# Kernel optimization log

Measured on AMD Instinct MI355X. Metric: run time of the kernel, lower is better.

Reference implementation:

```python
import jax, jax.numpy as jnp
import numpy as np

EMB_DIM = 1024
NUM_HEADS = 16
DEPTH = EMB_DIM // NUM_HEADS
B, LQ, LKV = 2, 1024, 2048


def setup_inputs() -> dict:
    key = jax.random.key(0)
    ks = jax.random.split(key, 8)
    s = 1.0 / np.sqrt(EMB_DIM)
    return {
        "x": jax.random.normal(ks[0], (B, LQ, EMB_DIM), jnp.float32),
        "context": jax.random.normal(ks[1], (B, LKV, EMB_DIM), jnp.float32),
        "pad_mask": jax.random.bernoulli(ks[2], 0.1, (B, LQ, LKV)),
        "Wq": jax.random.normal(ks[3], (EMB_DIM, EMB_DIM), jnp.float32) * s,
        "Wk": jax.random.normal(ks[4], (EMB_DIM, EMB_DIM), jnp.float32) * s,
        "Wv": jax.random.normal(ks[5], (EMB_DIM, EMB_DIM), jnp.float32) * s,
        "fc_w": jax.random.normal(ks[6], (EMB_DIM, EMB_DIM), jnp.float32) * s,
        "fc_b": jax.random.normal(ks[7], (EMB_DIM,), jnp.float32) * s,
    }


def reference(x, context, pad_mask, Wq, Wk, Wv, fc_w, fc_b):
    # Projections (torch Linear: y = x @ W.T)
    Q = jnp.einsum("bqe,fe->bqf", x, Wq)
    K = jnp.einsum("bke,fe->bkf", context, Wk)
    V = jnp.einsum("bke,fe->bkf", context, Wv)
    # Split heads: [B, H, L, D]
    Q = Q.reshape(B, LQ, NUM_HEADS, DEPTH).transpose(0, 2, 1, 3)
    K = K.reshape(B, LKV, NUM_HEADS, DEPTH).transpose(0, 2, 1, 3)
    V = V.reshape(B, LKV, NUM_HEADS, DEPTH).transpose(0, 2, 1, 3)
    # Scaled dot-product attention scores [B, H, LQ, LKV]
    scores = jnp.einsum("bhqd,bhkd->bhqk", Q, K) / np.sqrt(DEPTH).astype(np.float32)
    scores = jnp.where(pad_mask[:, None, :, :], jnp.float32(-1e9), scores)
    att = jax.nn.softmax(scores, axis=-1)
    out = jnp.einsum("bhqk,bhkd->bhqd", att, V)
    out = out.transpose(0, 2, 1, 3).reshape(B, LQ, EMB_DIM)
    return jnp.einsum("bqe,fe->bqf", out, fc_w) + fc_b
```

## Files before the change

kernel.cpp:

```cpp
#include <hip/hip_runtime.h>
#include <hip/hip_bf16.h>

#define B_   2
#define H_   16
#define LQ_  1024
#define LKV_ 2048
#define D_   64
#define E_   1024

typedef __attribute__((ext_vector_type(8))) _Float16 f16x8;
typedef __attribute__((ext_vector_type(4))) float   f32x4;

__device__ __forceinline__ void gload16_lds(const void* g, void* l) {
    __builtin_amdgcn_global_load_lds(
        (const __attribute__((address_space(1))) unsigned int*)g,
        (__attribute__((address_space(3))) unsigned int*)l, 16, 0, 0);
}

__global__ void probe16(const void* __restrict__ msk, int* __restrict__ modep) {
    int lane = threadIdx.x;
    int notInt = 0, notF32 = 0, notBF = 0;
    for (int i = lane; i < 256; i += 64) {
        unsigned v = ((const unsigned*)msk)[i * 997];
        if (v > 1u) notInt = 1;
        if (v != 0u && v != 0x3F800000u) notF32 = 1;
        if (v != 0u && v != 0x3F80u && v != 0x3F800000u && v != 0x3F803F80u) notBF = 1;
    }
    notInt = __any(notInt); notF32 = __any(notF32); notBF = __any(notBF);
    if (lane == 0) *modep = !notInt ? 0 : (!notF32 ? 1 : (!notBF ? 2 : 3));
}

__global__ void canon16_all(
    const float* __restrict__ x,  const float* __restrict__ ctx,
    const float* __restrict__ wq, const float* __restrict__ wk,
    const float* __restrict__ wv, const float* __restrict__ fw,
    const float* __restrict__ fb, const void* __restrict__ msk,
    _Float16* __restrict__ xh,  _Float16* __restrict__ ch,
    _Float16* __restrict__ wqh, _Float16* __restrict__ wkvh,
    _Float16* __restrict__ fwh, float* __restrict__ fbf,
    unsigned long long* __restrict__ Mbt, const int* __restrict__ modep)
{
    const int mmode = *modep;
    const int total = 1376384;
    const int stride = gridDim.x * blockDim.x;
    for (int idx = blockIdx.x * blockDim.x + threadIdx.x; idx < total; idx += stride) {
        if (idx < 1310720) {
            const float* src; _Float16* dst; int rel;
            if (idx < 262144)       { src = x;   dst = xh;   rel = idx; }
            else if (idx < 786432)  { src = ctx; dst = ch;   rel = idx - 262144; }
            else if (idx < 917504)  { src = wq;  dst = wqh;  rel = idx - 786432; }
            else if (idx < 1048576) { src = wk;  dst = wkvh; rel = idx - 917504; }
            else if (idx < 1179648) { src = wv;  dst = wkvh + (size_t)E_ * E_; rel = idx - 1048576; }
            else                    { src = fw;  dst = fwh;  rel = idx - 1179648; }
            f32x4 a = ((const f32x4*)src)[2 * rel], b = ((const f32x4*)src)[2 * rel + 1];
            f16x8 o;
            o[0] = (_Float16)a.x; o[1] = (_Float16)a.y; o[2] = (_Float16)a.z; o[3] = (_Float16)a.w;
            o[4] = (_Float16)b.x; o[5] = (_Float16)b.y; o[6] = (_Float16)b.z; o[7] = (_Float16)b.w;
            ((f16x8*)dst)[rel] = o;
        } else if (idx < 1310848) {
            int rel = idx - 1310720;
#pragma unroll
            for (int j = 0; j < 8; ++j) fbf[rel * 8 + j] = fb[rel * 8 + j];
        } else {
            int rel = idx - 1310848;
            const size_t base = (size_t)rel * 64;
            unsigned long long v = 0;
            if (mmode == 0) {
                const int* p = (const int*)msk + base;
#pragma unroll
                for (int j = 0; j < 64; ++j) if (p[j] != 0) v |= 1ull << j;
            } else if (mmode == 1) {
                const float* p = (const float*)msk + base;
#pragma unroll
                for (int j = 0; j < 64; ++j) if (p[j] != 0.0f) v |= 1ull << j;
            } else if (mmode == 2) {
                const unsigned short* p = (const unsigned short*)msk + base;
#pragma unroll
                for (int j = 0; j < 64; ++j) if (p[j] != 0) v |= 1ull << j;
            } else {
                const unsigned char* p = (const unsigned char*)msk + base;
#pragma unroll
                for (int j = 0; j < 64; ++j) if (p[j] != 0) v |= 1ull << j;
            }
            Mbt[(rel & 31) * 2048 + (rel >> 5)] = v;
        }
    }
}

__global__ __launch_bounds__(256) void gemm16_qkv(
    const _Float16* __restrict__ xh, const _Float16* __restrict__ ch,
    const _Float16* __restrict__ wqh, const _Float16* __restrict__ wkvh,
    _Float16* __restrict__ Qh, _Float16* __restrict__ Kh, _Float16* __restrict__ Vt)
{
    __shared__ __align__(16) _Float16 As[2][128 * 64];
    __shared__ __align__(16) _Float16 Bs[2][128 * 64];

    const int bid = blockIdx.x;
    const bool isQ = bid < 128;
    const _Float16* A; const _Float16* W; int tm, tn;
    if (isQ) { A = xh; W = wqh; tm = bid >> 3; tn = bid & 7; }
    else     { int b2 = bid - 128; A = ch; W = wkvh; tm = b2 >> 4; tn = b2 & 15; }

    const int tid = threadIdx.x;
    const int w = tid >> 6, lane = tid & 63;
    const int g = lane >> 4, c = lane & 15;
    const int wr = w >> 1, wc = w & 1;
    const int rowS = lane >> 3, slot = lane & 7;
    const int stSwz = ((slot ^ (rowS & 7)) << 4);
    const int swz0 = ((g ^ (c & 7)) << 4);
    const int swz1 = (((4 + g) ^ (c & 7)) << 4);

    f32x4 acc[4][4];
#pragma unroll
    for (int i = 0; i < 4; i++)
#pragma unroll
        for (int j = 0; j < 4; j++) acc[i][j] = f32x4{0.f, 0.f, 0.f, 0.f};

    const size_t rowB = (size_t)E_ * 2;
    const char* gAbase = (const char*)A + (size_t)(tm * 128) * rowB;
    const char* gBbase = (const char*)W + (size_t)(tn * 128) * rowB;

#pragma unroll
    for (int j = 0; j < 4; ++j) {
        int rloc = w * 32 + j * 8 + rowS;
        gload16_lds(gAbase + (size_t)rloc * rowB + stSwz,
                    (char*)As[0] + (w * 32 + j * 8) * 128 + lane * 16);
        gload16_lds(gBbase + (size_t)rloc * rowB + stSwz,
                    (char*)Bs[0] + (w * 32 + j * 8) * 128 + lane * 16);
    }
    __syncthreads();

    for (int kt = 0; kt < 16; ++kt) {
        if (kt < 15) {
            const int nb = (kt + 1) & 1;
#pragma unroll
            for (int j = 0; j < 4; ++j) {
                int rloc = w * 32 + j * 8 + rowS;
                gload16_lds(gAbase + (size_t)rloc * rowB + (kt + 1) * 128 + stSwz,
                            (char*)As[nb] + (w * 32 + j * 8) * 128 + lane * 16);
                gload16_lds(gBbase + (size_t)rloc * rowB + (kt + 1) * 128 + stSwz,
                            (char*)Bs[nb] + (w * 32 + j * 8) * 128 + lane * 16);
            }
        }
        const int cb = kt & 1;

        f16x8 bF[4][2];
#pragma unroll
        for (int ni = 0; ni < 4; ni++) {
            const char* bp = (const char*)Bs[cb] + (wc * 64 + ni * 16 + c) * 128;
            bF[ni][0] = *(const f16x8*)(bp + swz0);
            bF[ni][1] = *(const f16x8*)(bp + swz1);
        }
#pragma unroll
        for (int mi = 0; mi < 4; mi++) {
            const char* ap = (const char*)As[cb] + (wr * 64 + mi * 16 + c) * 128;
            f16x8 a0 = *(const f16x8*)(ap + swz0);
            f16x8 a1 = *(const f16x8*)(ap + swz1);
#pragma unroll
            for (int ni = 0; ni < 4; ni++) {
                acc[mi][ni] = __builtin_amdgcn_mfma_f32_16x16x32_f16(a0, bF[ni][0], acc[mi][ni], 0, 0, 0);
                acc[mi][ni] = __builtin_amdgcn_mfma_f32_16x16x32_f16(a1, bF[ni][1], acc[mi][ni], 0, 0, 0);
            }
        }
        __syncthreads();
    }

#pragma unroll
    for (int mi = 0; mi < 4; mi++) {
#pragma unroll
        for (int ni = 0; ni < 4; ni++) {
#pragma unroll
            for (int r = 0; r < 4; r++) {
                int R  = tm * 128 + wr * 64 + mi * 16 + g * 4 + r;
                int Cc = tn * 128 + wc * 64 + ni * 16 + c;
                float v = acc[mi][ni][r];
                if (isQ) {
                    int b = R >> 10, q = R & 1023;
                    int h = Cc >> 6, d = Cc & 63;
                    Qh[((size_t)(b * H_ + h) * LQ_ + q) * D_ + d] = (_Float16)(v * 0.18033688011112042f);
                } else {
                    int b = R >> 11, k = R & 2047;
                    int isV = Cc >> 10, cc2 = Cc & 1023;
                    int h = cc2 >> 6, d = cc2 & 63;
                    if (!isV)
                        Kh[((size_t)(b * H_ + h) * LKV_ + k) * D_ + d] = (_Float16)v;
                    else {
                        size_t bh = (size_t)(b * H_ + h);
                        Vt[((bh * (LKV_ / 64) + (k >> 6)) * D_ + d) * 64 + (k & 63)] = (_Float16)v;
                    }
                }
            }
        }
    }
}

__global__ __launch_bounds__(256) void gemm16_fc(
    const _Float16* __restrict__ A, const _Float16* __restrict__ W,
    const float* __restrict__ bias, float* __restrict__ Cout)
{
    __shared__ __align__(16) _Float16 As[2][128 * 64];
    __shared__ __align__(16) _Float16 Bs[2][128 * 64];

    const int tm = blockIdx.x >> 3, tn = blockIdx.x & 7;
    const int tid = threadIdx.x;
    const int w = tid >> 6, lane = tid & 63;
    const int g = lane >> 4, c = lane & 15;
    const int wr = w >> 1, wc = w & 1;
    const int rowS = lane >> 3, slot = lane & 7;
    const int stSwz = ((slot ^ (rowS & 7)) << 4);
    const int swz0 = ((g ^ (c & 7)) << 4);
    const int swz1 = (((4 + g) ^ (c & 7)) << 4);

    f32x4 acc[4][4];
#pragma unroll
    for (int i = 0; i < 4; i++)
#pragma unroll
        for (int j = 0; j < 4; j++) acc[i][j] = f32x4{0.f, 0.f, 0.f, 0.f};

    const size_t rowB = (size_t)E_ * 2;
    const char* gAbase = (const char*)A + (size_t)(tm * 128) * rowB;
    const char* gBbase = (const char*)W + (size_t)(tn * 128) * rowB;

#pragma unroll
    for (int j = 0; j < 4; ++j) {
        int rloc = w * 32 + j * 8 + rowS;
        gload16_lds(gAbase + (size_t)rloc * rowB + stSwz,
                    (char*)As[0] + (w * 32 + j * 8) * 128 + lane * 16);
        gload16_lds(gBbase + (size_t)rloc * rowB + stSwz,
                    (char*)Bs[0] + (w * 32 + j * 8) * 128 + lane * 16);
    }
    __syncthreads();

    for (int kt = 0; kt < 16; ++kt) {
        if (kt < 15) {
            const int nb = (kt + 1) & 1;
#pragma unroll
            for (int j = 0; j < 4; ++j) {
                int rloc = w * 32 + j * 8 + rowS;
                gload16_lds(gAbase + (size_t)rloc * rowB + (kt + 1) * 128 + stSwz,
                            (char*)As[nb] + (w * 32 + j * 8) * 128 + lane * 16);
                gload16_lds(gBbase + (size_t)rloc * rowB + (kt + 1) * 128 + stSwz,
                            (char*)Bs[nb] + (w * 32 + j * 8) * 128 + lane * 16);
            }
        }
        const int cb = kt & 1;

        f16x8 bF[4][2];
#pragma unroll
        for (int ni = 0; ni < 4; ni++) {
            const char* bp = (const char*)Bs[cb] + (wc * 64 + ni * 16 + c) * 128;
            bF[ni][0] = *(const f16x8*)(bp + swz0);
            bF[ni][1] = *(const f16x8*)(bp + swz1);
        }
#pragma unroll
        for (int mi = 0; mi < 4; mi++) {
            const char* ap = (const char*)As[cb] + (wr * 64 + mi * 16 + c) * 128;
            f16x8 a0 = *(const f16x8*)(ap + swz0);
            f16x8 a1 = *(const f16x8*)(ap + swz1);
#pragma unroll
            for (int ni = 0; ni < 4; ni++) {
                acc[mi][ni] = __builtin_amdgcn_mfma_f32_16x16x32_f16(a0, bF[ni][0], acc[mi][ni], 0, 0, 0);
                acc[mi][ni] = __builtin_amdgcn_mfma_f32_16x16x32_f16(a1, bF[ni][1], acc[mi][ni], 0, 0, 0);
            }
        }
        __syncthreads();
    }

#pragma unroll
    for (int mi = 0; mi < 4; mi++)
#pragma unroll
        for (int ni = 0; ni < 4; ni++)
#pragma unroll
            for (int r = 0; r < 4; r++) {
                int R  = tm * 128 + wr * 64 + mi * 16 + g * 4 + r;
                int Cc = tn * 128 + wc * 64 + ni * 16 + c;
                Cout[(size_t)R * E_ + Cc] = acc[mi][ni][r] + bias[Cc];
            }
}

__global__ __launch_bounds__(512) void attn16_kernel(
    const _Float16* __restrict__ Qh,
    const _Float16* __restrict__ Kh,
    const _Float16* __restrict__ Vt,
    const unsigned long long* __restrict__ Mbt,
    _Float16* __restrict__ O)
{
    __shared__ __align__(16) char ldsraw[65536];

    const int bid0 = blockIdx.x;
    const int xcd = bid0 & 7, jj = bid0 >> 3;
    const int bh = xcd * 4 + (jj >> 4);
    const int qt = jj & 15;
    const int b = bh >> 4, h = bh & 15;
    const int tid = threadIdx.x;
    const int w = tid >> 6, lane = tid & 63;
    const int g = lane >> 4, c = lane & 15;
    const int ws = w >> 2, wq = w & 3;
    const int q0 = qt * 64 + wq * 16;

    char* half = ldsraw + ws * 32768;

    f16x8 qf[2];
#pragma unroll
    for (int ks = 0; ks < 2; ++ks)
        qf[ks] = *(const f16x8*)&Qh[((size_t)bh * LQ_ + q0 + c) * D_ + ks * 32 + g * 8];

    f32x4 o[4];
#pragma unroll
    for (int dt = 0; dt < 4; dt++) o[dt] = f32x4{0.f, 0.f, 0.f, 0.f};
    float m = -1e30f, lsum = 0.f;

    const int rowS = (lane >> 3);
    const int stOffBase = (rowS * 128) + (((lane & 7) ^ (rowS & 7)) * 16);
    const char* kTileB = (const char*)Kh + (size_t)bh * (LKV_ * D_ * 2) + (size_t)ws * 16 * 8192;
    const char* vTileB = (const char*)Vt + (size_t)bh * (LKV_ * D_ * 2) + (size_t)ws * 16 * 8192;

    int rdOff[2];
#pragma unroll
    for (int ks = 0; ks < 2; ++ks)
        rdOff[ks] = c * 128 + (((ks * 4 + g) ^ (c & 7)) * 16);

    const int srcLo = (((g & 1) << 1) * 16 + c) << 2;
    const int srcHi = ((((g & 1) << 1) + 1) * 16 + c) << 2;
    const bool hiSel = (g >= 2);

    const int mRowIdx = b * LQ_ + q0 + c;
    const size_t mTile0 = (size_t)(ws * 16) * 2048 + mRowIdx;

    {
#pragma unroll
        for (int j = 0; j < 2; ++j) {
            gload16_lds(kTileB + (wq * 2048 + j * 1024) + stOffBase, half + (wq * 2048 + j * 1024));
            gload16_lds(vTileB + (wq * 2048 + j * 1024) + stOffBase, half + 8192 + (wq * 2048 + j * 1024));
        }
    }
    __syncthreads();

    for (int t = 0; t < 16; ++t) {
        if (t < 15) {
            const char* kt = kTileB + (size_t)(t + 1) * 8192;
            const char* vt = vTileB + (size_t)(t + 1) * 8192;
            char* dst = half + ((t + 1) & 1) * 16384;
#pragma unroll
            for (int j = 0; j < 2; ++j) {
                gload16_lds(kt + (wq * 2048 + j * 1024) + stOffBase, dst + (wq * 2048 + j * 1024));
                gload16_lds(vt + (wq * 2048 + j * 1024) + stOffBase, dst + 8192 + (wq * 2048 + j * 1024));
            }
        }

        const char* bufp = half + (t & 1) * 16384;

        f32x4 s[4];
#pragma unroll
        for (int nt = 0; nt < 4; ++nt) {
            f32x4 accS = f32x4{0.f, 0.f, 0.f, 0.f};
#pragma unroll
            for (int ks = 0; ks < 2; ++ks) {
                f16x8 kf = *(const f16x8*)(bufp + nt * 2048 + rdOff[ks]);
                accS = __builtin_amdgcn_mfma_f32_16x16x32_f16(kf, qf[ks], accS, 0, 0, 0);
            }
            s[nt] = accS;
        }
        unsigned long long mks = Mbt[mTile0 + (size_t)t * 2048] >> (g * 4);
#pragma unroll
        for (int nt = 0; nt < 4; ++nt) {
            unsigned nib = (unsigned)(mks >> (nt * 16)) & 0xFu;
            if (nib & 1u) s[nt][0] = -1e9f;
            if (nib & 2u) s[nt][1] = -1e9f;
            if (nib & 4u) s[nt][2] = -1e9f;
            if (nib & 8u) s[nt][3] = -1e9f;
        }
        float t0 = fmaxf(fmaxf(s[0][0], s[0][1]), fmaxf(s[0][2], s[0][3]));
        float t1 = fmaxf(fmaxf(s[1][0], s[1][1]), fmaxf(s[1][2], s[1][3]));
        float t2 = fmaxf(fmaxf(s[2][0], s[2][1]), fmaxf(s[2][2], s[2][3]));
        float t3 = fmaxf(fmaxf(s[3][0], s[3][1]), fmaxf(s[3][2], s[3][3]));
        float tmax = fmaxf(fmaxf(t0, t1), fmaxf(t2, t3));
        tmax = fmaxf(tmax, __shfl_xor(tmax, 16, 64));
        tmax = fmaxf(tmax, __shfl_xor(tmax, 32, 64));
        if (!__all(tmax - m <= 8.0f)) {
            float mn = fmaxf(m, tmax);
            float scl = exp2f(m - mn);
            m = mn;
            lsum *= scl;
#pragma unroll
            for (int dt = 0; dt < 4; dt++)
#pragma unroll
                for (int r = 0; r < 4; r++) o[dt][r] *= scl;
        }
        float ts = 0.f;
#pragma unroll
        for (int nt = 0; nt < 4; ++nt) {
            float p0 = exp2f(s[nt][0] - m);
            float p1 = exp2f(s[nt][1] - m);
            float p2 = exp2f(s[nt][2] - m);
            float p3 = exp2f(s[nt][3] - m);
            s[nt][0] = p0; s[nt][1] = p1; s[nt][2] = p2; s[nt][3] = p3;
            ts += (p0 + p1) + (p2 + p3);
        }
        ts += __shfl_xor(ts, 16, 64);
        ts += __shfl_xor(ts, 32, 64);
        lsum += ts;
        int pk[4][2];
#pragma unroll
        for (int nt = 0; nt < 4; ++nt) {
            pk[nt][0] = __builtin_bit_cast(int, __builtin_amdgcn_cvt_pkrtz(s[nt][0], s[nt][1]));
            pk[nt][1] = __builtin_bit_cast(int, __builtin_amdgcn_cvt_pkrtz(s[nt][2], s[nt][3]));
        }
#pragma unroll
        for (int ks = 0; ks < 2; ++ks) {
            const int ntL = 2 * ks, ntH = 2 * ks + 1;
            int aL0 = __builtin_amdgcn_ds_bpermute(srcLo, pk[ntL][0]);
            int aL1 = __builtin_amdgcn_ds_bpermute(srcLo, pk[ntL][1]);
            int aH0 = __builtin_amdgcn_ds_bpermute(srcHi, pk[ntL][0]);
            int aH1 = __builtin_amdgcn_ds_bpermute(srcHi, pk[ntL][1]);
            int bL0 = __builtin_amdgcn_ds_bpermute(srcLo, pk[ntH][0]);
            int bL1 = __builtin_amdgcn_ds_bpermute(srcLo, pk[ntH][1]);
            int bH0 = __builtin_amdgcn_ds_bpermute(srcHi, pk[ntH][0]);
            int bH1 = __builtin_amdgcn_ds_bpermute(srcHi, pk[ntH][1]);
            int u[4];
            u[0] = hiSel ? bL0 : aL0;
            u[1] = hiSel ? bL1 : aL1;
            u[2] = hiSel ? bH0 : aH0;
            u[3] = hiSel ? bH1 : aH1;
            f16x8 pf;
            {
                union { int i[4]; f16x8 v; } cvt;
                cvt.i[0] = u[0]; cvt.i[1] = u[1]; cvt.i[2] = u[2]; cvt.i[3] = u[3];
                pf = cvt.v;
            }
#pragma unroll
            for (int dt = 0; dt < 4; ++dt) {
                f16x8 vf = *(const f16x8*)(bufp + 8192 + dt * 2048 + rdOff[ks]);
                o[dt] = __builtin_amdgcn_mfma_f32_16x16x32_f16(vf, pf, o[dt], 0, 0, 0);
            }
        }
        __syncthreads();
    }

    float* OfP = (float*)ldsraw;
    float* Ml  = (float*)(ldsraw + 34816);
#pragma unroll
    for (int dt = 0; dt < 4; ++dt)
#pragma unroll
        for (int r = 0; r < 4; r++)
            OfP[(w * 16 + c) * 68 + dt * 16 + 4 * g + r] = o[dt][r];
    if (lane < 16) {
        Ml[(w * 16 + lane) * 2 + 0] = m;
        Ml[(w * 16 + lane) * 2 + 1] = lsum;
    }
    __syncthreads();

    const int d = tid & 63;
    const int qlBase = tid >> 6;
#pragma unroll
    for (int pass = 0; pass < 8; ++pass) {
        int ql = pass * 8 + qlBase;
        float m0 = Ml[ql * 2], l0 = Ml[ql * 2 + 1];
        float m1 = Ml[(64 + ql) * 2], l1 = Ml[(64 + ql) * 2 + 1];
        float M  = fmaxf(m0, m1);
        float e0 = exp2f(m0 - M), e1 = exp2f(m1 - M);
        float L  = l0 * e0 + l1 * e1;
        float acc = OfP[ql * 68 + d] * e0 + OfP[(64 + ql) * 68 + d] * e1;
        O[((size_t)b * LQ_ + qt * 64 + ql) * E_ + h * 64 + d] = (_Float16)(acc / L);
    }
}

extern "C" void kernel_launch(void* const* d_in, const int* in_sizes, int n_in,
                              void* d_out, int out_size, void* d_ws, size_t ws_size,
                              hipStream_t stream)
{
    const float* x   = (const float*)d_in[0];
    const float* ctx = (const float*)d_in[1];
    const void*  msk = d_in[2];
    const float* Wq  = (const float*)d_in[3];
    const float* Wk  = (const float*)d_in[4];
    const float* Wv  = (const float*)d_in[5];
    const float* fcw = (const float*)d_in[6];
    const float* fcb = (const float*)d_in[7];
    float* out = (float*)d_out;

    char* ws = (char*)d_ws;
    size_t off = 0;
    auto alloc = [&](size_t bytes) { char* p = ws + off; off += (bytes + 255) & ~255ull; return p; };

    int* modep = (int*)alloc(256);
    unsigned long long* Mbt = (unsigned long long*)alloc((size_t)B_ * LQ_ * (LKV_ / 64) * 8);
    _Float16* xh   = (_Float16*)alloc((size_t)B_ * LQ_ * E_ * 2);
    _Float16* ch   = (_Float16*)alloc((size_t)B_ * LKV_ * E_ * 2);
    _Float16* wqh  = (_Float16*)alloc((size_t)E_ * E_ * 2);
    _Float16* wkvh = (_Float16*)alloc((size_t)2 * E_ * E_ * 2);
    _Float16* fwh  = (_Float16*)alloc((size_t)E_ * E_ * 2);
    float*    fbf  = (float*)alloc((size_t)E_ * 4);
    _Float16* Qh   = (_Float16*)alloc((size_t)B_ * H_ * LQ_ * D_ * 2);
    _Float16* Kh   = (_Float16*)alloc((size_t)B_ * H_ * LKV_ * D_ * 2);
    _Float16* Vt   = (_Float16*)alloc((size_t)B_ * H_ * LKV_ * D_ * 2);
    _Float16* Ob   = xh;
    (void)ws_size; (void)in_sizes; (void)n_in; (void)out_size;

    probe16<<<1, 64, 0, stream>>>(msk, modep);

    canon16_all<<<2048, 256, 0, stream>>>(x, ctx, Wq, Wk, Wv, fcw, fcb, msk,
                                          xh, ch, wqh, wkvh, fwh, fbf, Mbt, modep);

    gemm16_qkv<<<640, 256, 0, stream>>>(xh, ch, wqh, wkvh, Qh, Kh, Vt);

    attn16_kernel<<<512, 512, 0, stream>>>(Qh, Kh, Vt, Mbt, Ob);

    gemm16_fc<<<128, 256, 0, stream>>>(Ob, fwh, fbf, out);
}
```

Measured before the change: 143.1 us.

## Split attention KV range across separate blocks with global combine kernel

```diff
diff --git a/kernel.cpp b/kernel.cpp
--- a/kernel.cpp
+++ b/kernel.cpp
@@ -9,15 +9,25 @@
 #define E_   1024
 
 typedef __attribute__((ext_vector_type(8))) _Float16 f16x8;
+typedef __attribute__((ext_vector_type(4))) _Float16 f16x4;
 typedef __attribute__((ext_vector_type(4))) float   f32x4;
+typedef __attribute__((ext_vector_type(4))) unsigned short u16x4;
 
 __device__ __forceinline__ void gload16_lds(const void* g, void* l) {
     __builtin_amdgcn_global_load_lds(
         (const __attribute__((address_space(1))) unsigned int*)g,
         (__attribute__((address_space(3))) unsigned int*)l, 16, 0, 0);
 }
-
-__global__ void probe16(const void* __restrict__ msk, int* __restrict__ modep) {
+__device__ __forceinline__ unsigned short f2bf(float f) {
+    union { float f; unsigned u; } v; v.f = f;
+    unsigned r = v.u + 0x7FFFu + ((v.u >> 16) & 1u);
+    return (unsigned short)(r >> 16);
+}
+__device__ __forceinline__ float bf2f(unsigned short u) {
+    union { unsigned u; float f; } v; v.u = ((unsigned)u) << 16; return v.f;
+}
+
+__global__ void probe17(const void* __restrict__ msk, int* __restrict__ modep) {
     int lane = threadIdx.x;
     int notInt = 0, notF32 = 0, notBF = 0;
     for (int i = lane; i < 256; i += 64) {
@@ -30,7 +40,7 @@
     if (lane == 0) *modep = !notInt ? 0 : (!notF32 ? 1 : (!notBF ? 2 : 3));
 }
 
-__global__ void canon16_all(
+__global__ void canon17_all(
     const float* __restrict__ x,  const float* __restrict__ ctx,
     const float* __restrict__ wq, const float* __restrict__ wk,
     const float* __restrict__ wv, const float* __restrict__ fw,
@@ -87,7 +97,7 @@
     }
 }
 
-__global__ __launch_bounds__(256) void gemm16_qkv(
+__global__ __launch_bounds__(256) void gemm17_qkv(
     const _Float16* __restrict__ xh, const _Float16* __restrict__ ch,
     const _Float16* __restrict__ wqh, const _Float16* __restrict__ wkvh,
     _Float16* __restrict__ Qh, _Float16* __restrict__ Kh, _Float16* __restrict__ Vt)
@@ -194,7 +204,7 @@
     }
 }
 
-__global__ __launch_bounds__(256) void gemm16_fc(
+__global__ __launch_bounds__(256) void gemm17_fc(
     const _Float16* __restrict__ A, const _Float16* __restrict__ W,
     const float* __restrict__ bias, float* __restrict__ Cout)
 {
@@ -278,27 +288,26 @@
             }
 }
 
-__global__ __launch_bounds__(512) void attn16_kernel(
+__global__ __launch_bounds__(256) void attn17_kernel(
     const _Float16* __restrict__ Qh,
     const _Float16* __restrict__ Kh,
     const _Float16* __restrict__ Vt,
     const unsigned long long* __restrict__ Mbt,
-    _Float16* __restrict__ O)
+    unsigned short* __restrict__ Opart,
+    float* __restrict__ Ml2)
 {
-    __shared__ __align__(16) char ldsraw[65536];
+    __shared__ __align__(16) char ldsraw[32768];
 
     const int bid0 = blockIdx.x;
     const int xcd = bid0 & 7, jj = bid0 >> 3;
-    const int bh = xcd * 4 + (jj >> 4);
-    const int qt = jj & 15;
-    const int b = bh >> 4, h = bh & 15;
+    const int bh = xcd * 4 + (jj >> 5);
+    const int rem = jj & 31;
+    const int qt = rem >> 1, ksHalf = rem & 1;
+    const int b = bh >> 4, h = bh & 15; (void)h; (void)b;
     const int tid = threadIdx.x;
     const int w = tid >> 6, lane = tid & 63;
     const int g = lane >> 4, c = lane & 15;
-    const int ws = w >> 2, wq = w & 3;
-    const int q0 = qt * 64 + wq * 16;
-
-    char* half = ldsraw + ws * 32768;
+    const int q0 = qt * 64 + w * 16;
 
     f16x8 qf[2];
 #pragma unroll
@@ -312,8 +321,8 @@
 
     const int rowS = (lane >> 3);
     const int stOffBase = (rowS * 128) + (((lane & 7) ^ (rowS & 7)) * 16);
-    const char* kTileB = (const char*)Kh + (size_t)bh * (LKV_ * D_ * 2) + (size_t)ws * 16 * 8192;
-    const char* vTileB = (const char*)Vt + (size_t)bh * (LKV_ * D_ * 2) + (size_t)ws * 16 * 8192;
+    const char* kTileB = (const char*)Kh + (size_t)bh * (LKV_ * D_ * 2) + (size_t)ksHalf * 16 * 8192;
+    const char* vTileB = (const char*)Vt + (size_t)bh * (LKV_ * D_ * 2) + (size_t)ksHalf * 16 * 8192;
 
     int rdOff[2];
 #pragma unroll
@@ -324,14 +333,14 @@
     const int srcHi = ((((g & 1) << 1) + 1) * 16 + c) << 2;
     const bool hiSel = (g >= 2);
 
-    const int mRowIdx = b * LQ_ + q0 + c;
-    const size_t mTile0 = (size_t)(ws * 16) * 2048 + mRowIdx;
+    const int mRowIdx = (bh >> 4) * LQ_ + q0 + c;
+    const size_t mTile0 = (size_t)(ksHalf * 16) * 2048 + mRowIdx;
 
     {
 #pragma unroll
         for (int j = 0; j < 2; ++j) {
-            gload16_lds(kTileB + (wq * 2048 + j * 1024) + stOffBase, half + (wq * 2048 + j * 1024));
-            gload16_lds(vTileB + (wq * 2048 + j * 1024) + stOffBase, half + 8192 + (wq * 2048 + j * 1024));
+            gload16_lds(kTileB + (w * 2048 + j * 1024) + stOffBase, ldsraw + (w * 2048 + j * 1024));
+            gload16_lds(vTileB + (w * 2048 + j * 1024) + stOffBase, ldsraw + 8192 + (w * 2048 + j * 1024));
         }
     }
     __syncthreads();
@@ -340,15 +349,15 @@
         if (t < 15) {
             const char* kt = kTileB + (size_t)(t + 1) * 8192;
             const char* vt = vTileB + (size_t)(t + 1) * 8192;
-            char* dst = half + ((t + 1) & 1) * 16384;
+            char* dst = ldsraw + ((t + 1) & 1) * 16384;
 #pragma unroll
             for (int j = 0; j < 2; ++j) {
-                gload16_lds(kt + (wq * 2048 + j * 1024) + stOffBase, dst + (wq * 2048 + j * 1024));
-                gload16_lds(vt + (wq * 2048 + j * 1024) + stOffBase, dst + 8192 + (wq * 2048 + j * 1024));
-            }
-        }
-
-        const char* bufp = half + (t & 1) * 16384;
+                gload16_lds(kt + (w * 2048 + j * 1024) + stOffBase, dst + (w * 2048 + j * 1024));
+                gload16_lds(vt + (w * 2048 + j * 1024) + stOffBase, dst + 8192 + (w * 2048 + j * 1024));
+            }
+        }
+
+        const char* bufp = ldsraw + (t & 1) * 16384;
 
         f32x4 s[4];
 #pragma unroll
@@ -437,32 +446,45 @@
         __syncthreads();
     }
 
-    float* OfP = (float*)ldsraw;
-    float* Ml  = (float*)(ldsraw + 34816);
-#pragma unroll
-    for (int dt = 0; dt < 4; ++dt)
-#pragma unroll
-        for (int r = 0; r < 4; r++)
-            OfP[(w * 16 + c) * 68 + dt * 16 + 4 * g + r] = o[dt][r];
+    unsigned short* opBase = Opart + (((size_t)(ksHalf * 32 + bh) * LQ_ + (q0 + c)) * D_);
+#pragma unroll
+    for (int dt = 0; dt < 4; ++dt) {
+        u16x4 pv;
+#pragma unroll
+        for (int r = 0; r < 4; ++r) pv[r] = f2bf(o[dt][r]);
+        *(u16x4*)(opBase + dt * 16 + 4 * g) = pv;
+    }
     if (lane < 16) {
-        Ml[(w * 16 + lane) * 2 + 0] = m;
-        Ml[(w * 16 + lane) * 2 + 1] = lsum;
-    }
-    __syncthreads();
-
-    const int d = tid & 63;
-    const int qlBase = tid >> 6;
-#pragma unroll
-    for (int pass = 0; pass < 8; ++pass) {
-        int ql = pass * 8 + qlBase;
-        float m0 = Ml[ql * 2], l0 = Ml[ql * 2 + 1];
-        float m1 = Ml[(64 + ql) * 2], l1 = Ml[(64 + ql) * 2 + 1];
-        float M  = fmaxf(m0, m1);
-        float e0 = exp2f(m0 - M), e1 = exp2f(m1 - M);
-        float L  = l0 * e0 + l1 * e1;
-        float acc = OfP[ql * 68 + d] * e0 + OfP[(64 + ql) * 68 + d] * e1;
-        O[((size_t)b * LQ_ + qt * 64 + ql) * E_ + h * 64 + d] = (_Float16)(acc / L);
-    }
+        float* mlp = Ml2 + ((size_t)(ksHalf * 32 + bh) * LQ_ + (q0 + lane)) * 2;
+        mlp[0] = m;
+        mlp[1] = lsum;
+    }
+}
+
+__global__ __launch_bounds__(256) void combine17(
+    const unsigned short* __restrict__ Opart,
+    const float* __restrict__ Ml2,
+    _Float16* __restrict__ O)
+{
+    int idx = blockIdx.x * 256 + threadIdx.x;
+    int bh = idx >> 14;
+    int q  = (idx >> 4) & 1023;
+    int d4 = idx & 15;
+    const float* ml0 = Ml2 + ((size_t)bh * LQ_ + q) * 2;
+    const float* ml1 = Ml2 + ((size_t)(32 + bh) * LQ_ + q) * 2;
+    float m0 = ml0[0], l0 = ml0[1];
+    float m1 = ml1[0], l1 = ml1[1];
+    float M  = fmaxf(m0, m1);
+    float e0 = exp2f(m0 - M), e1 = exp2f(m1 - M);
+    float inv = 1.0f / (l0 * e0 + l1 * e1);
+    u16x4 a = *(const u16x4*)(Opart + ((size_t)bh * LQ_ + q) * D_ + d4 * 4);
+    u16x4 bq = *(const u16x4*)(Opart + ((size_t)(32 + bh) * LQ_ + q) * D_ + d4 * 4);
+    f16x4 outv;
+#pragma unroll
+    for (int j = 0; j < 4; ++j)
+        outv[j] = (_Float16)((bf2f(a[j]) * e0 + bf2f(bq[j]) * e1) * inv);
+    int b = bh >> 4, h = bh & 15;
+    *(f16x4*)&O[((size_t)(b * LQ_ + q)) * E_ + h * 64 + d4 * 4] = outv;
 }
 
 extern "C" void kernel_launch(void* const* d_in, const int* in_sizes, int n_in,
@@ -495,16 +517,20 @@
     _Float16* Kh   = (_Float16*)alloc((size_t)B_ * H_ * LKV_ * D_ * 2);
     _Float16* Vt   = (_Float16*)alloc((size_t)B_ * H_ * LKV_ * D_ * 2);
     _Float16* Ob   = xh;
+    unsigned short* Opart = (unsigned short*)ch;
+    float* Ml2 = (float*)wqh;
     (void)ws_size; (void)in_sizes; (void)n_in; (void)out_size;
 
-    probe16<<<1, 64, 0, stream>>>(msk, modep);
-
-    canon16_all<<<2048, 256, 0, stream>>>(x, ctx, Wq, Wk, Wv, fcw, fcb, msk,
+    probe17<<<1, 64, 0, stream>>>(msk, modep);
+
+    canon17_all<<<2048, 256, 0, stream>>>(x, ctx, Wq, Wk, Wv, fcw, fcb, msk,
                                           xh, ch, wqh, wkvh, fwh, fbf, Mbt, modep);
 
-    gemm16_qkv<<<640, 256, 0, stream>>>(xh, ch, wqh, wkvh, Qh, Kh, Vt);
-
-    attn16_kernel<<<512, 512, 0, stream>>>(Qh, Kh, Vt, Mbt, Ob);
-
-    gemm16_fc<<<128, 256, 0, stream>>>(Ob, fwh, fbf, out);
-}
+    gemm17_qkv<<<640, 256, 0, stream>>>(xh, ch, wqh, wkvh, Qh, Kh, Vt);
+
+    attn17_kernel<<<1024, 256, 0, stream>>>(Qh, Kh, Vt, Mbt, Opart, Ml2);
+
+    combine17<<<2048, 256, 0, stream>>>(Opart, Ml2, Ob);
+
+    gemm17_fc<<<128, 256, 0, stream>>>(Ob, fwh, fbf, out);
+}
```

Result: slower. 149.0 us (+4.1%).
